# Kernel tuning notes

Hardware: AMD Instinct MI355X
Metric: run time of the kernel (lower is better)

The kernel has to match this reference:

```python
import jax, jax.numpy as jnp
import numpy as np

RHO = 1e-8
EPS = 1e-8
THRESH = 0.9
MARK = -2


def maxi(x):
    # keep only the max entry along last dim, zero elsewhere
    idx = jnp.argmax(x, axis=-1, keepdims=True)
    return jnp.where(jnp.arange(x.shape[-1]) == idx, x, 0.0)


def argmaxi(x, eps=EPS):
    mx = jnp.abs(maxi(x))
    factors = jnp.max(mx, axis=-1, keepdims=True) - eps
    return mx / factors


def outer_forward(mm0, xs, rho=RHO):
    # mm0: (fields, mems, dim), xs: (batch, fields, dim)
    m = mm0 - 0.5
    x = xs - 0.5
    num = jnp.einsum('fmd,bfd->bfm', m, x) * 0.5
    m_norm = jnp.sqrt(jnp.sum(m * m, axis=-1))            # (f, m)
    x_norm = jnp.sqrt(jnp.sum(x * x, axis=-1))[..., None]  # (b, f, 1)
    return num / (m_norm[None] * x_norm + rho) + 0.5


def hidden_forward(mm, child_x, rho=RHO):
    # mm: (nodes, children, h_mems, c_mems), child_x: (batch, nodes*children, c_mems)
    n, c, hm, cm = mm.shape
    b = child_x.shape[0]
    x = maxi(child_x).reshape(b, n, c, cm)
    prop = jnp.einsum('nchk,bnck->bnh', mm, x)
    x_norm = jnp.sqrt(jnp.sum(x * x, axis=(2, 3)))[..., None]  # (b, n, 1)
    return prop / (c * x_norm + rho)


def mark_reserved_indices(acts, usages, trigger, mark=MARK):
    # acts: (b, n, m); usages: (n, m); trigger: (b, n, 1)
    res = jnp.argsort(acts, axis=-1)[:, :, -1:]        # argmax index, (b, n, 1)
    res = jnp.where(trigger, -1, res)
    res = res[:, :, 0].T                               # (n, b)
    sort_indices = jnp.argsort(usages, axis=-1)        # (n, m) ascending usage
    mask = res != -1                                   # (n, b)
    matches = ((res[:, :, None] == sort_indices[:, None, :]) & mask[:, :, None]).any(axis=1)  # (n, m)
    return jnp.where(matches, mark, sort_indices), sort_indices


def move_value_to_back(x, value=MARK):
    order = jnp.argsort((x == value).astype(jnp.int32), axis=-1)  # stable sort
    return jnp.take_along_axis(x, order, axis=-1)


def expand_for_batches(x, batch_size):
    n, m = x.shape
    full = batch_size // m + 1
    tiled = jnp.broadcast_to(x[None], (full, n, m)).transpose(1, 0, 2).reshape(n, -1)
    return tiled[:, :batch_size]


def growth_argmaxi(x, counts, eps=EPS, threshold=THRESH):
    b, n, m = x.shape
    normal = argmaxi(x, eps)
    trigger = jnp.sum(x > threshold, axis=-1, keepdims=True) <= 0  # (b, n, 1)
    avail, allidx = mark_reserved_indices(normal, counts, trigger, MARK)
    avail = move_value_to_back(avail, MARK)
    avail = expand_for_batches(avail, b)
    allidx = expand_for_batches(allidx, b)
    final = jnp.where(avail == MARK, allidx, avail)  # (n, b)
    idx = final.T.reshape(b, n, 1)
    vals = jnp.take_along_axis(x, idx, axis=-1)
    vals = jnp.where(vals == 0, 1.0, vals)
    gp = jnp.where(jnp.arange(m) == idx, vals, 0.0)  # scatter into zeros
    gp = argmaxi(jnp.abs(gp), eps)
    grown = jnp.where(trigger, gp, normal)
    uc = jnp.sum(grown, axis=0)
    uc = jnp.where(uc <= 0, counts, uc)
    return grown, uc


def setup_inputs() -> dict:
    key = jax.random.key(0)
    k1, k2, k3, k4 = jax.random.split(key, 4)
    xs = jax.random.uniform(k1, (32, 4096, 64), dtype=jnp.float32)
    mm0 = jax.random.uniform(k2, (4096, 64, 64), dtype=jnp.float32)
    mm1 = jax.random.normal(k3, (512, 8, 64, 64), dtype=jnp.float32) * 0.1
    mm2 = jax.random.normal(k4, (64, 8, 64, 64), dtype=jnp.float32) * 0.1
    counts = jnp.ones((64, 64), dtype=jnp.float32)
    return {'xs': xs, 'mm0': mm0, 'mm1': mm1, 'mm2': mm2, 'counts': counts}


def reference(xs, mm0, mm1, mm2, counts):
    h0 = outer_forward(mm0, xs)      # (b, 4096, 64)
    h1 = hidden_forward(mm1, h0)     # (b, 512, 64)
    h2 = hidden_forward(mm2, h1)     # (b, 64, 64)
    grown, _ = growth_argmaxi(h2, counts)
    return grown
```

## Files before the change

### kernel.cpp

```cpp
#include <hip/hip_runtime.h>
#include <cstdint>
#include <cstddef>

#define RHO 1e-8f
#define EPSV 1e-8f
#define THRESH 0.9f

typedef float v2f __attribute__((ext_vector_type(2)));

__device__ __forceinline__ float wave_max(float v) {
#pragma unroll
  for (int off = 1; off < 64; off <<= 1) v = fmaxf(v, __shfl_xor(v, off, 64));
  return v;
}

__global__ __launch_bounds__(128) void stage1_kernel(
    const float* __restrict__ xs, const float* __restrict__ mm0,
    float* __restrict__ maxv1, int* __restrict__ idx1) {
  const int tid = threadIdx.x;
  const int lane = tid & 63;
  const int wave = tid >> 6;
  const int f = blockIdx.x;

  __shared__ float mS[64 * 64];
  __shared__ float xS[32 * 64];
  __shared__ float mnS[64];
  __shared__ float xnS[32];
  __shared__ float bestS[2][32];
  __shared__ int bidxS[2][32];

  const float* mf = mm0 + (size_t)f * 4096;
#pragma unroll
  for (int i = 0; i < 8; ++i) {
    const int g = tid + 128 * i;
    const int r = g >> 4, q = g & 15;
    float4 v = *reinterpret_cast<const float4*>(mf + g * 4);
    float4 w = {v.x - 0.5f, v.y - 0.5f, v.z - 0.5f, v.w - 0.5f};
    *reinterpret_cast<float4*>(&mS[(r * 16 + (q ^ (r & 15))) * 4]) = w;
  }
  const float* xf = xs + (size_t)f * 64;
#pragma unroll
  for (int i = 0; i < 4; ++i) {
    const int g = tid + 128 * i;
    const int b = g >> 4, q = g & 15;
    float4 v = *reinterpret_cast<const float4*>(xf + (size_t)b * (4096 * 64) + q * 4);
    float4 w = {v.x - 0.5f, v.y - 0.5f, v.z - 0.5f, v.w - 0.5f};
    *reinterpret_cast<float4*>(&xS[(b * 16 + (q ^ (b & 15))) * 4]) = w;
  }
  __syncthreads();

  if (tid < 96) {
    const int r = (tid < 64) ? tid : (tid - 64);
    const float* base = (tid < 64) ? mS : xS;
    v2f s = {0.f, 0.f};
#pragma unroll
    for (int q = 0; q < 16; ++q) {
      float4 v = *reinterpret_cast<const float4*>(&base[(r * 16 + (q ^ (r & 15))) * 4]);
      s = (v2f){v.x, v.y} * (v2f){v.x, v.y} + s;
      s = (v2f){v.z, v.w} * (v2f){v.z, v.w} + s;
    }
    const float n = sqrtf(s.x + s.y);
    if (tid < 64) mnS[r] = n; else xnS[r] = n;
  }
  __syncthreads();

  const int mg = lane >> 3, bg = lane & 7;
  const int mrow0 = wave * 32 + mg;
  v2f acc[4][4][2];
#pragma unroll
  for (int i = 0; i < 4; ++i)
#pragma unroll
    for (int j = 0; j < 4; ++j) {
      acc[i][j][0] = (v2f){0.f, 0.f};
      acc[i][j][1] = (v2f){0.f, 0.f};
    }

#pragma unroll
  for (int d0 = 0; d0 < 64; d0 += 4) {
    const int q = d0 >> 2;
    float4 a[4], bx[4];
#pragma unroll
    for (int i = 0; i < 4; ++i) {
      const int r = mrow0 + 8 * i;
      a[i] = *reinterpret_cast<const float4*>(&mS[(r * 16 + (q ^ (r & 15))) * 4]);
    }
#pragma unroll
    for (int j = 0; j < 4; ++j) {
      const int b = bg + 8 * j;
      bx[j] = *reinterpret_cast<const float4*>(&xS[(b * 16 + (q ^ (b & 15))) * 4]);
    }
#pragma unroll
    for (int i = 0; i < 4; ++i)
#pragma unroll
      for (int j = 0; j < 4; ++j) {
        acc[i][j][0] = (v2f){a[i].x, a[i].y} * (v2f){bx[j].x, bx[j].y} + acc[i][j][0];
        acc[i][j][1] = (v2f){a[i].z, a[i].w} * (v2f){bx[j].z, bx[j].w} + acc[i][j][1];
      }
  }

  float mn_i[4], xn_j[4];
#pragma unroll
  for (int i = 0; i < 4; ++i) mn_i[i] = mnS[mrow0 + 8 * i];
#pragma unroll
  for (int j = 0; j < 4; ++j) xn_j[j] = xnS[bg + 8 * j];

  float best[4];
  int bidx[4];
#pragma unroll
  for (int j = 0; j < 4; ++j) { best[j] = -__builtin_inff(); bidx[j] = 0; }
#pragma unroll
  for (int i = 0; i < 4; ++i)
#pragma unroll
    for (int j = 0; j < 4; ++j) {
      const float dot =
          acc[i][j][0].x + acc[i][j][0].y + acc[i][j][1].x + acc[i][j][1].y;
      const float val = (dot * 0.5f) / (mn_i[i] * xn_j[j] + RHO) + 0.5f;
      if (val > best[j]) { best[j] = val; bidx[j] = mrow0 + 8 * i; }
    }
#pragma unroll
  for (int off = 8; off < 64; off <<= 1) {
#pragma unroll
    for (int j = 0; j < 4; ++j) {
      const float pv = __shfl_xor(best[j], off, 64);
      const int pm = __shfl_xor(bidx[j], off, 64);
      if (pv > best[j] || (pv == best[j] && pm < bidx[j])) {
        best[j] = pv; bidx[j] = pm;
      }
    }
  }
  if (mg == 0) {
#pragma unroll
    for (int j = 0; j < 4; ++j) {
      bestS[wave][bg + 8 * j] = best[j];
      bidxS[wave][bg + 8 * j] = bidx[j];
    }
  }
  __syncthreads();
  if (tid < 32) {
    const float v0 = bestS[0][tid], v1 = bestS[1][tid];
    const int i0 = bidxS[0][tid], i1 = bidxS[1][tid];
    const bool take1 = (v1 > v0);
    maxv1[f * 32 + tid] = take1 ? v1 : v0;
    idx1[f * 32 + tid] = take1 ? i1 : i0;
  }
}

#define STAGE_WRITE(T, R)                                    \
  do {                                                       \
    _Pragma("unroll") for (int i_ = 0; i_ < 4; ++i_) {       \
      const int g_ = tid + 256 * i_;                         \
      const int h_ = g_ >> 4, k0_ = (g_ & 15) * 4;           \
      (T)[(k0_ + 0) * 64 + (h_ ^ (k0_ + 0))] = (R)[i_].x;    \
      (T)[(k0_ + 1) * 64 + (h_ ^ (k0_ + 1))] = (R)[i_].y;    \
      (T)[(k0_ + 2) * 64 + (h_ ^ (k0_ + 2))] = (R)[i_].z;    \
      (T)[(k0_ + 3) * 64 + (h_ ^ (k0_ + 3))] = (R)[i_].w;    \
    }                                                        \
  } while (0)

#define LOAD_CHILD(R, C)                                     \
  do {                                                       \
    _Pragma("unroll") for (int i_ = 0; i_ < 4; ++i_)         \
        (R)[i_] = src[(C) * 1024 + tid + 256 * i_];          \
  } while (0)

#define COMPUTE_CHILD(C, T)                                              \
  do {                                                                   \
    _Pragma("unroll") for (int i_ = 0; i_ < 8; ++i_) {                   \
      const int b_ = wave * 8 + i_;                                      \
      const int k_ = ixL[(C) * 32 + b_];                                 \
      const float v_ = mvL[(C) * 32 + b_];                               \
      const float w_ = (T)[k_ * 64 + (lane ^ k_)];                       \
      acc[i_] = fmaf(w_, v_, acc[i_]);                                   \
      s2[i_] = fmaf(v_, v_, s2[i_]);                                     \
    }                                                                    \
  } while (0)

__global__ __launch_bounds__(256) void stage2_kernel(
    const float* __restrict__ maxv_in, const int* __restrict__ idx_in,
    const float* __restrict__ mm,
    float* __restrict__ maxv_out, int* __restrict__ idx_out) {
  const int node = blockIdx.x;
  const int lane = threadIdx.x & 63;
  const int wave = threadIdx.x >> 6;
  const int tid = threadIdx.x;

  __shared__ float tA[4096], tB[4096];
  __shared__ float mvL[256];
  __shared__ int ixL[256];

  const float4* src = reinterpret_cast<const float4*>(mm + (size_t)node * (8 * 4096));

  mvL[tid] = maxv_in[node * 256 + tid];
  ixL[tid] = idx_in[node * 256 + tid];

  float acc[8], s2[8];
#pragma unroll
  for (int i = 0; i < 8; ++i) { acc[i] = 0.f; s2[i] = 0.f; }

  float4 rE[4], rO[4];
  LOAD_CHILD(rE, 0);
  LOAD_CHILD(rO, 1);
  STAGE_WRITE(tA, rE);
  __syncthreads();

#pragma unroll
  for (int cc = 0; cc < 8; cc += 2) {
    if (cc + 2 < 8) LOAD_CHILD(rE, cc + 2);
    COMPUTE_CHILD(cc, tA);
    STAGE_WRITE(tB, rO);
    __syncthreads();
    if (cc + 3 < 8) LOAD_CHILD(rO, cc + 3);
    COMPUTE_CHILD(cc + 1, tB);
    if (cc + 2 < 8) {
      STAGE_WRITE(tA, rE);
    }
    __syncthreads();
  }

#pragma unroll
  for (int i = 0; i < 8; ++i) {
    const int b = wave * 8 + i;
    const float val = acc[i] / (8.f * sqrtf(s2[i]) + RHO);
    const float mx = wave_max(val);
    unsigned long long t = __ballot(val == mx);
    int j0 = __ffsll((long long)t) - 1;
    if (lane == 0) {
      maxv_out[node * 32 + b] = mx;
      idx_out[node * 32 + b] = j0;
    }
  }
}

__global__ __launch_bounds__(256) void grow_kernel(
    const float* __restrict__ maxv_in, const int* __restrict__ idx_in,
    const float* __restrict__ mm,
    const float* __restrict__ counts, float* __restrict__ out) {
  const int node = blockIdx.x;
  const int lane = threadIdx.x & 63;
  const int wave = threadIdx.x >> 6;
  const int tid = threadIdx.x;

  __shared__ float tA[4096], tB[4096];
  __shared__ float mvL[256];
  __shared__ int ixL[256];
  __shared__ float hbuf[32 * 64];
  __shared__ float mxvS[32];
  __shared__ int idxS[32];
  __shared__ int trgS[32];
  __shared__ float cntS[64];
  __shared__ int sidxS[64];
  __shared__ int flagS[64];
  __shared__ int compS[64];
  __shared__ int selS[32];
  __shared__ float valS[32];
  __shared__ int keptS[1];

  const float4* src = reinterpret_cast<const float4*>(mm + (size_t)node * (8 * 4096));

  mvL[tid] = maxv_in[node * 256 + tid];
  ixL[tid] = idx_in[node * 256 + tid];

  float acc[8], s2[8];
#pragma unroll
  for (int i = 0; i < 8; ++i) { acc[i] = 0.f; s2[i] = 0.f; }

  float4 rE[4], rO[4];
  LOAD_CHILD(rE, 0);
  LOAD_CHILD(rO, 1);
  STAGE_WRITE(tA, rE);
  __syncthreads();

#pragma unroll
  for (int cc = 0; cc < 8; cc += 2) {
    if (cc + 2 < 8) LOAD_CHILD(rE, cc + 2);
    COMPUTE_CHILD(cc, tA);
    STAGE_WRITE(tB, rO);
    __syncthreads();
    if (cc + 3 < 8) LOAD_CHILD(rO, cc + 3);
    COMPUTE_CHILD(cc + 1, tB);
    if (cc + 2 < 8) {
      STAGE_WRITE(tA, rE);
    }
    __syncthreads();
  }

#pragma unroll
  for (int i = 0; i < 8; ++i) {
    const int b = wave * 8 + i;
    const float val = acc[i] / (8.f * sqrtf(s2[i]) + RHO);
    const float mx = wave_max(val);
    unsigned long long t = __ballot(val == mx);
    int j0 = __ffsll((long long)t) - 1;
    hbuf[b * 64 + lane] = val;
    unsigned long long big = __ballot(val > THRESH);
    if (lane == 0) {
      mxvS[b] = mx; idxS[b] = j0; trgS[b] = (big == 0ULL) ? 1 : 0;
    }
  }

  if (tid < 64) { cntS[tid] = counts[node * 64 + tid]; flagS[tid] = 0; }
  __syncthreads();
  if (tid < 64) {
    float cl = cntS[tid];
    int rank = 0;
    for (int j = 0; j < 64; ++j) {
      float cj = cntS[j];
      rank += (cj < cl || (cj == cl && j < tid)) ? 1 : 0;
    }
    sidxS[rank] = tid;
  }
  __syncthreads();
  if (tid < 32) {
    const int b = tid;
    if (!trgS[b]) {
      int j = idxS[b];
      float a = fabsf(mxvS[b]);
      int res;
      if (a > EPSV) res = j;
      else if (a == 0.f) res = 63;
      else if (a == EPSV) res = j;
      else res = (j == 63) ? 62 : 63;
      flagS[res] = 1;
    }
  }
  __syncthreads();
  if (wave == 0) {
    int s = sidxS[lane];
    int keep = flagS[s] ? 0 : 1;
    unsigned long long kb = __ballot(keep);
    int pos = __popcll(kb & ((1ULL << lane) - 1ULL));
    if (keep) compS[pos] = s;
    if (lane == 0) keptS[0] = __popcll(kb);
  }
  __syncthreads();
  if (tid < 32) {
    const int b = tid;
    int fin = (b < keptS[0]) ? compS[b] : sidxS[b];
    int idxb; float a;
    if (trgS[b]) {
      idxb = fin;
      float v = hbuf[b * 64 + idxb];
      if (v == 0.f) v = 1.f;
      a = fabsf(v);
    } else {
      idxb = idxS[b];
      a = fabsf(mxvS[b]);
    }
    selS[b] = idxb;
    valS[b] = a / (a - EPSV);
  }
  __syncthreads();
#pragma unroll
  for (int r = 0; r < 8; ++r) {
    int i = tid + 256 * r;
    int b = i >> 6, h = i & 63;
    out[((size_t)b * 64 + node) * 64 + h] = (h == selS[b]) ? valS[b] : 0.f;
  }
}

extern "C" void kernel_launch(void* const* d_in, const int* in_sizes, int n_in,
                              void* d_out, int out_size, void* d_ws, size_t ws_size,
                              hipStream_t stream) {
  const float* xs = (const float*)d_in[0];
  const float* mm0 = (const float*)d_in[1];
  const float* mm1 = (const float*)d_in[2];
  const float* mm2 = (const float*)d_in[3];
  const float* counts = (const float*)d_in[4];
  float* out = (float*)d_out;
  char* ws = (char*)d_ws;

  float* maxv1 = (float*)(ws + 0);
  int* idx1 = (int*)(ws + 524288);
  float* maxv2 = (float*)(ws + 1048576);
  int* idx2 = (int*)(ws + 1114112);

  stage1_kernel<<<dim3(4096), dim3(128), 0, stream>>>(xs, mm0, maxv1, idx1);
  stage2_kernel<<<dim3(512), dim3(256), 0, stream>>>(maxv1, idx1, mm1, maxv2, idx2);
  grow_kernel<<<dim3(64), dim3(256), 0, stream>>>(maxv2, idx2, mm2, counts, out);
}
```

Baseline: 205.9 us.

## Read stage1 operands directly from global memory and use LDS-only barriers

```diff
diff --git a/kernel.cpp b/kernel.cpp
--- a/kernel.cpp
+++ b/kernel.cpp
@@ -12,6 +12,13 @@
 #pragma unroll
   for (int off = 1; off < 64; off <<= 1) v = fmaxf(v, __shfl_xor(v, off, 64));
   return v;
+}
+
+__device__ __forceinline__ void lds_barrier() {
+  asm volatile("s_waitcnt lgkmcnt(0)" ::: "memory");
+  __builtin_amdgcn_sched_barrier(0);
+  __builtin_amdgcn_s_barrier();
+  __builtin_amdgcn_sched_barrier(0);
 }
 
 __global__ __launch_bounds__(128) void stage1_kernel(
@@ -21,73 +28,51 @@
   const int lane = tid & 63;
   const int wave = tid >> 6;
   const int f = blockIdx.x;
-
-  __shared__ float mS[64 * 64];
-  __shared__ float xS[32 * 64];
-  __shared__ float mnS[64];
-  __shared__ float xnS[32];
+  const int mg = lane >> 3, bg = lane & 7;
+  const int mrow0 = wave * 32 + mg;
+
   __shared__ float bestS[2][32];
   __shared__ int bidxS[2][32];
 
-  const float* mf = mm0 + (size_t)f * 4096;
-#pragma unroll
-  for (int i = 0; i < 8; ++i) {
-    const int g = tid + 128 * i;
-    const int r = g >> 4, q = g & 15;
-    float4 v = *reinterpret_cast<const float4*>(mf + g * 4);
-    float4 w = {v.x - 0.5f, v.y - 0.5f, v.z - 0.5f, v.w - 0.5f};
-    *reinterpret_cast<float4*>(&mS[(r * 16 + (q ^ (r & 15))) * 4]) = w;
-  }
-  const float* xf = xs + (size_t)f * 64;
+  const float* mb = mm0 + (size_t)f * 4096 + (size_t)mrow0 * 64;
+  const float* xb = xs + (size_t)f * 64 + (size_t)bg * (4096 * 64);
+
+  v2f acc[4][4][2];
+  v2f na[4], nx[4];
 #pragma unroll
   for (int i = 0; i < 4; ++i) {
-    const int g = tid + 128 * i;
-    const int b = g >> 4, q = g & 15;
-    float4 v = *reinterpret_cast<const float4*>(xf + (size_t)b * (4096 * 64) + q * 4);
-    float4 w = {v.x - 0.5f, v.y - 0.5f, v.z - 0.5f, v.w - 0.5f};
-    *reinterpret_cast<float4*>(&xS[(b * 16 + (q ^ (b & 15))) * 4]) = w;
-  }
-  __syncthreads();
-
-  if (tid < 96) {
-    const int r = (tid < 64) ? tid : (tid - 64);
-    const float* base = (tid < 64) ? mS : xS;
-    v2f s = {0.f, 0.f};
-#pragma unroll
-    for (int q = 0; q < 16; ++q) {
-      float4 v = *reinterpret_cast<const float4*>(&base[(r * 16 + (q ^ (r & 15))) * 4]);
-      s = (v2f){v.x, v.y} * (v2f){v.x, v.y} + s;
-      s = (v2f){v.z, v.w} * (v2f){v.z, v.w} + s;
-    }
-    const float n = sqrtf(s.x + s.y);
-    if (tid < 64) mnS[r] = n; else xnS[r] = n;
-  }
-  __syncthreads();
-
-  const int mg = lane >> 3, bg = lane & 7;
-  const int mrow0 = wave * 32 + mg;
-  v2f acc[4][4][2];
-#pragma unroll
-  for (int i = 0; i < 4; ++i)
+    na[i] = (v2f){0.f, 0.f};
+    nx[i] = (v2f){0.f, 0.f};
 #pragma unroll
     for (int j = 0; j < 4; ++j) {
       acc[i][j][0] = (v2f){0.f, 0.f};
       acc[i][j][1] = (v2f){0.f, 0.f};
     }
-
-#pragma unroll
-  for (int d0 = 0; d0 < 64; d0 += 4) {
-    const int q = d0 >> 2;
+  }
+
+#pragma clang loop unroll_count(2)
+  for (int q = 0; q < 16; ++q) {
     float4 a[4], bx[4];
 #pragma unroll
     for (int i = 0; i < 4; ++i) {
-      const int r = mrow0 + 8 * i;
-      a[i] = *reinterpret_cast<const float4*>(&mS[(r * 16 + (q ^ (r & 15))) * 4]);
-    }
-#pragma unroll
-    for (int j = 0; j < 4; ++j) {
-      const int b = bg + 8 * j;
-      bx[j] = *reinterpret_cast<const float4*>(&xS[(b * 16 + (q ^ (b & 15))) * 4]);
+      float4 v = *reinterpret_cast<const float4*>(mb + i * (8 * 64) + 4 * q);
+      a[i] = (float4){v.x - 0.5f, v.y - 0.5f, v.z - 0.5f, v.w - 0.5f};
+    }
+#pragma unroll
+    for (int j = 0; j < 4; ++j) {
+      float4 v = *reinterpret_cast<const float4*>(
+          xb + (size_t)j * (8 * 4096 * 64) + 4 * q);
+      bx[j] = (float4){v.x - 0.5f, v.y - 0.5f, v.z - 0.5f, v.w - 0.5f};
+    }
+#pragma unroll
+    for (int i = 0; i < 4; ++i) {
+      na[i] = (v2f){a[i].x, a[i].y} * (v2f){a[i].x, a[i].y} + na[i];
+      na[i] = (v2f){a[i].z, a[i].w} * (v2f){a[i].z, a[i].w} + na[i];
+    }
+#pragma unroll
+    for (int j = 0; j < 4; ++j) {
+      nx[j] = (v2f){bx[j].x, bx[j].y} * (v2f){bx[j].x, bx[j].y} + nx[j];
+      nx[j] = (v2f){bx[j].z, bx[j].w} * (v2f){bx[j].z, bx[j].w} + nx[j];
     }
 #pragma unroll
     for (int i = 0; i < 4; ++i)
@@ -100,9 +85,9 @@
 
   float mn_i[4], xn_j[4];
 #pragma unroll
-  for (int i = 0; i < 4; ++i) mn_i[i] = mnS[mrow0 + 8 * i];
-#pragma unroll
-  for (int j = 0; j < 4; ++j) xn_j[j] = xnS[bg + 8 * j];
+  for (int i = 0; i < 4; ++i) mn_i[i] = sqrtf(na[i].x + na[i].y);
+#pragma unroll
+  for (int j = 0; j < 4; ++j) xn_j[j] = sqrtf(nx[j].x + nx[j].y);
 
   float best[4];
   int bidx[4];
@@ -175,6 +160,25 @@
     }                                                                    \
   } while (0)
 
+#define PIPELINE_MATMUL()                        \
+  do {                                           \
+    float4 rE[4], rO[4];                         \
+    LOAD_CHILD(rE, 0);                           \
+    LOAD_CHILD(rO, 1);                           \
+    STAGE_WRITE(tA, rE);                         \
+    lds_barrier();                               \
+    _Pragma("unroll") for (int cc = 0; cc < 8; cc += 2) { \
+      if (cc + 2 < 8) LOAD_CHILD(rE, cc + 2);    \
+      COMPUTE_CHILD(cc, tA);                     \
+      STAGE_WRITE(tB, rO);                       \
+      lds_barrier();                             \
+      if (cc + 3 < 8) LOAD_CHILD(rO, cc + 3);    \
+      COMPUTE_CHILD(cc + 1, tB);                 \
+      if (cc + 2 < 8) { STAGE_WRITE(tA, rE); }   \
+      lds_barrier();                             \
+    }                                            \
+  } while (0)
+
 __global__ __launch_bounds__(256) void stage2_kernel(
     const float* __restrict__ maxv_in, const int* __restrict__ idx_in,
     const float* __restrict__ mm,
@@ -197,25 +201,7 @@
 #pragma unroll
   for (int i = 0; i < 8; ++i) { acc[i] = 0.f; s2[i] = 0.f; }
 
-  float4 rE[4], rO[4];
-  LOAD_CHILD(rE, 0);
-  LOAD_CHILD(rO, 1);
-  STAGE_WRITE(tA, rE);
-  __syncthreads();
-
-#pragma unroll
-  for (int cc = 0; cc < 8; cc += 2) {
-    if (cc + 2 < 8) LOAD_CHILD(rE, cc + 2);
-    COMPUTE_CHILD(cc, tA);
-    STAGE_WRITE(tB, rO);
-    __syncthreads();
-    if (cc + 3 < 8) LOAD_CHILD(rO, cc + 3);
-    COMPUTE_CHILD(cc + 1, tB);
-    if (cc + 2 < 8) {
-      STAGE_WRITE(tA, rE);
-    }
-    __syncthreads();
-  }
+  PIPELINE_MATMUL();
 
 #pragma unroll
   for (int i = 0; i < 8; ++i) {
@@ -264,25 +250,7 @@
 #pragma unroll
   for (int i = 0; i < 8; ++i) { acc[i] = 0.f; s2[i] = 0.f; }
 
-  float4 rE[4], rO[4];
-  LOAD_CHILD(rE, 0);
-  LOAD_CHILD(rO, 1);
-  STAGE_WRITE(tA, rE);
-  __syncthreads();
-
-#pragma unroll
-  for (int cc = 0; cc < 8; cc += 2) {
-    if (cc + 2 < 8) LOAD_CHILD(rE, cc + 2);
-    COMPUTE_CHILD(cc, tA);
-    STAGE_WRITE(tB, rO);
-    __syncthreads();
-    if (cc + 3 < 8) LOAD_CHILD(rO, cc + 3);
-    COMPUTE_CHILD(cc + 1, tB);
-    if (cc + 2 < 8) {
-      STAGE_WRITE(tA, rE);
-    }
-    __syncthreads();
-  }
+  PIPELINE_MATMUL();
 
 #pragma unroll
   for (int i = 0; i < 8; ++i) {
```

Result: slower. 247.3 us (+20.1%).

## Gather only selected weight rows instead of staging full child matrices

Applied to the files above, without the earlier changes.

```diff
diff --git a/kernel.cpp b/kernel.cpp
--- a/kernel.cpp
+++ b/kernel.cpp
@@ -145,89 +145,41 @@
   }
 }
 
-#define STAGE_WRITE(T, R)                                    \
-  do {                                                       \
-    _Pragma("unroll") for (int i_ = 0; i_ < 4; ++i_) {       \
-      const int g_ = tid + 256 * i_;                         \
-      const int h_ = g_ >> 4, k0_ = (g_ & 15) * 4;           \
-      (T)[(k0_ + 0) * 64 + (h_ ^ (k0_ + 0))] = (R)[i_].x;    \
-      (T)[(k0_ + 1) * 64 + (h_ ^ (k0_ + 1))] = (R)[i_].y;    \
-      (T)[(k0_ + 2) * 64 + (h_ ^ (k0_ + 2))] = (R)[i_].z;    \
-      (T)[(k0_ + 3) * 64 + (h_ ^ (k0_ + 3))] = (R)[i_].w;    \
-    }                                                        \
-  } while (0)
-
-#define LOAD_CHILD(R, C)                                     \
-  do {                                                       \
-    _Pragma("unroll") for (int i_ = 0; i_ < 4; ++i_)         \
-        (R)[i_] = src[(C) * 1024 + tid + 256 * i_];          \
-  } while (0)
-
-#define COMPUTE_CHILD(C, T)                                              \
-  do {                                                                   \
-    _Pragma("unroll") for (int i_ = 0; i_ < 8; ++i_) {                   \
-      const int b_ = wave * 8 + i_;                                      \
-      const int k_ = ixL[(C) * 32 + b_];                                 \
-      const float v_ = mvL[(C) * 32 + b_];                               \
-      const float w_ = (T)[k_ * 64 + (lane ^ k_)];                       \
-      acc[i_] = fmaf(w_, v_, acc[i_]);                                   \
-      s2[i_] = fmaf(v_, v_, s2[i_]);                                     \
-    }                                                                    \
-  } while (0)
-
 __global__ __launch_bounds__(256) void stage2_kernel(
     const float* __restrict__ maxv_in, const int* __restrict__ idx_in,
     const float* __restrict__ mm,
     float* __restrict__ maxv_out, int* __restrict__ idx_out) {
-  const int node = blockIdx.x;
   const int lane = threadIdx.x & 63;
   const int wave = threadIdx.x >> 6;
-  const int tid = threadIdx.x;
-
-  __shared__ float tA[4096], tB[4096];
-  __shared__ float mvL[256];
-  __shared__ int ixL[256];
-
-  const float4* src = reinterpret_cast<const float4*>(mm + (size_t)node * (8 * 4096));
-
-  mvL[tid] = maxv_in[node * 256 + tid];
-  ixL[tid] = idx_in[node * 256 + tid];
-
-  float acc[8], s2[8];
-#pragma unroll
-  for (int i = 0; i < 8; ++i) { acc[i] = 0.f; s2[i] = 0.f; }
-
-  float4 rE[4], rO[4];
-  LOAD_CHILD(rE, 0);
-  LOAD_CHILD(rO, 1);
-  STAGE_WRITE(tA, rE);
-  __syncthreads();
-
-#pragma unroll
-  for (int cc = 0; cc < 8; cc += 2) {
-    if (cc + 2 < 8) LOAD_CHILD(rE, cc + 2);
-    COMPUTE_CHILD(cc, tA);
-    STAGE_WRITE(tB, rO);
-    __syncthreads();
-    if (cc + 3 < 8) LOAD_CHILD(rO, cc + 3);
-    COMPUTE_CHILD(cc + 1, tB);
-    if (cc + 2 < 8) {
-      STAGE_WRITE(tA, rE);
-    }
-    __syncthreads();
-  }
-
-#pragma unroll
-  for (int i = 0; i < 8; ++i) {
-    const int b = wave * 8 + i;
-    const float val = acc[i] / (8.f * sqrtf(s2[i]) + RHO);
-    const float mx = wave_max(val);
-    unsigned long long t = __ballot(val == mx);
-    int j0 = __ffsll((long long)t) - 1;
-    if (lane == 0) {
-      maxv_out[node * 32 + b] = mx;
-      idx_out[node * 32 + b] = j0;
-    }
+  const int p = blockIdx.x * 4 + wave;
+  const int node = p >> 5;
+  const int b = p & 31;
+
+  int ks[8];
+  float vs[8];
+#pragma unroll
+  for (int c = 0; c < 8; ++c) {
+    const int off = __builtin_amdgcn_readfirstlane((node * 8 + c) * 32 + b);
+    ks[c] = idx_in[off];
+    vs[c] = maxv_in[off];
+  }
+
+  const float* wbase = mm + (size_t)node * (8 * 4096) + (size_t)lane * 64;
+  float acc = 0.f, s2 = 0.f;
+#pragma unroll
+  for (int c = 0; c < 8; ++c) {
+    const float w = wbase[c * 4096 + ks[c]];
+    acc = fmaf(w, vs[c], acc);
+    s2 = fmaf(vs[c], vs[c], s2);
+  }
+
+  const float val = acc / (8.f * sqrtf(s2) + RHO);
+  const float mx = wave_max(val);
+  unsigned long long t = __ballot(val == mx);
+  int j0 = __ffsll((long long)t) - 1;
+  if (lane == 0) {
+    maxv_out[node * 32 + b] = mx;
+    idx_out[node * 32 + b] = j0;
   }
 }
 
@@ -240,9 +192,6 @@
   const int wave = threadIdx.x >> 6;
   const int tid = threadIdx.x;
 
-  __shared__ float tA[4096], tB[4096];
-  __shared__ float mvL[256];
-  __shared__ int ixL[256];
   __shared__ float hbuf[32 * 64];
   __shared__ float mxvS[32];
   __shared__ int idxS[32];
@@ -255,33 +204,24 @@
   __shared__ float valS[32];
   __shared__ int keptS[1];
 
-  const float4* src = reinterpret_cast<const float4*>(mm + (size_t)node * (8 * 4096));
-
-  mvL[tid] = maxv_in[node * 256 + tid];
-  ixL[tid] = idx_in[node * 256 + tid];
+  const float* wbase = mm + (size_t)node * (8 * 4096) + (size_t)lane * 64;
 
   float acc[8], s2[8];
 #pragma unroll
   for (int i = 0; i < 8; ++i) { acc[i] = 0.f; s2[i] = 0.f; }
 
-  float4 rE[4], rO[4];
-  LOAD_CHILD(rE, 0);
-  LOAD_CHILD(rO, 1);
-  STAGE_WRITE(tA, rE);
-  __syncthreads();
-
-#pragma unroll
-  for (int cc = 0; cc < 8; cc += 2) {
-    if (cc + 2 < 8) LOAD_CHILD(rE, cc + 2);
-    COMPUTE_CHILD(cc, tA);
-    STAGE_WRITE(tB, rO);
-    __syncthreads();
-    if (cc + 3 < 8) LOAD_CHILD(rO, cc + 3);
-    COMPUTE_CHILD(cc + 1, tB);
-    if (cc + 2 < 8) {
-      STAGE_WRITE(tA, rE);
-    }
-    __syncthreads();
+#pragma unroll
+  for (int i = 0; i < 8; ++i) {
+    const int b = wave * 8 + i;
+#pragma unroll
+    for (int c = 0; c < 8; ++c) {
+      const int off = __builtin_amdgcn_readfirstlane((node * 8 + c) * 32 + b);
+      const int k = idx_in[off];
+      const float v = maxv_in[off];
+      const float w = wbase[c * 4096 + k];
+      acc[i] = fmaf(w, v, acc[i]);
+      s2[i] = fmaf(v, v, s2[i]);
+    }
   }
 
 #pragma unroll
@@ -375,6 +315,6 @@
   int* idx2 = (int*)(ws + 1114112);
 
   stage1_kernel<<<dim3(4096), dim3(128), 0, stream>>>(xs, mm0, maxv1, idx1);
-  stage2_kernel<<<dim3(512), dim3(256), 0, stream>>>(maxv1, idx1, mm1, maxv2, idx2);
+  stage2_kernel<<<dim3(4096), dim3(256), 0, stream>>>(maxv1, idx1, mm1, maxv2, idx2);
   grow_kernel<<<dim3(64), dim3(256), 0, stream>>>(maxv2, idx2, mm2, counts, out);
 }
```

Measured after the change: 256.4 us. 1.24x slower.
